# Performance work log

Hardware: AMD Instinct MI355X
Metric: run time of the kernel (lower is better)

The kernel has to match this reference:

```python
import jax, jax.numpy as jnp
import numpy as np

N_NODES = 500_000
N_EDGES = 5_000_000


def _glorot(key, shape):
    fan_in, fan_out = shape[0], shape[1]
    s = jnp.sqrt(6.0 / (fan_in + fan_out))
    return jax.random.uniform(key, shape, jnp.float32, -s, s)


def setup_inputs() -> dict:
    key = jax.random.key(0)
    ks = jax.random.split(key, 16)
    x = jax.random.normal(ks[0], (N_NODES, 3), jnp.float32)
    edge_index = jax.random.randint(ks[1], (2, N_EDGES), 0, N_NODES, jnp.int64)
    dims = [(3, 16), (16, 16), (16, 1)]
    inp = {"x": x, "edge_index": edge_index}
    for i, (din, dout) in enumerate(dims, start=1):
        k = jax.random.split(ks[1 + i], 5)
        inp[f"p{i}_w"] = _glorot(k[0], (din, din))   # project lin (bias=True)
        inp[f"p{i}_b"] = jnp.zeros((din,), jnp.float32)
        inp[f"l{i}_w"] = _glorot(k[1], (din, dout))  # lin_l on aggregated neighbors (bias=True)
        inp[f"l{i}_b"] = jnp.zeros((dout,), jnp.float32)
        inp[f"r{i}_w"] = _glorot(k[2], (din, dout))  # lin_r on root (bias=False)
    return inp


def _sage_conv(x, src, dst, pw, pb, lw, lb, rw):
    # project=True: neighbor messages use relu(lin(x)); root term uses original x
    h = jax.nn.relu(x @ pw + pb)                    # [N, din]
    msg = jnp.take(h, src, axis=0)                  # [E, din] gather from source j
    agg = jax.ops.segment_sum(msg, dst, num_segments=N_NODES)  # scatter-add to target i
    return agg @ lw + lb + x @ rw                   # [N, dout]


def reference(x, edge_index, p1_w, p1_b, l1_w, l1_b, r1_w,
              p2_w, p2_b, l2_w, l2_b, r2_w,
              p3_w, p3_b, l3_w, l3_b, r3_w):
    src, dst = edge_index[0], edge_index[1]
    h = jax.nn.relu(_sage_conv(x, src, dst, p1_w, p1_b, l1_w, l1_b, r1_w))
    h = jax.nn.relu(_sage_conv(h, src, dst, p2_w, p2_b, l2_w, l2_b, r2_w))
    return jax.nn.sigmoid(_sage_conv(h, src, dst, p3_w, p3_b, l3_w, l3_b, r3_w))
```

## Files before the change

### kernel.cpp

```cpp
#include <hip/hip_runtime.h>
#include <hip/hip_fp16.h>
#include <math.h>

#define NN 500000
#define NE 5000000
#define K_B 977
#define NBP 500
#define EPB 10000
#define CAP 6144
#define SEG 3072
#define PH 16
#define PHW 31250

__device__ inline float2 cvt2(unsigned u) {
    __half2 h = *reinterpret_cast<const __half2*>(&u);
    return __half22float2(h);
}

__device__ inline int wave_iscan(int x, int lane) {
#pragma unroll
    for (int d = 1; d < 64; d <<= 1) {
        int u = __shfl_up(x, d);
        if (lane >= d) x += u;
    }
    return x;
}


__global__ __launch_bounds__(512) void part_kernel(
    const int* __restrict__ ei, int* __restrict__ counts,
    unsigned int* __restrict__ edg_staged,
    const float* __restrict__ x, const float* __restrict__ p1w,
    const float* __restrict__ p1b, __half* __restrict__ h1)
{
    __shared__ unsigned stage[EPB];
    __shared__ int hist[1024];
    __shared__ int wsum[8];
    int t = threadIdx.x, j = blockIdx.x;
    int e0 = j * EPB;
    hist[t] = 0; hist[t + 512] = 0;
    __syncthreads();
    for (int k = t; k < EPB; k += 512) {
        int d = ei[NE + e0 + k];
        atomicAdd(&hist[d >> 9], 1);
    }
    __syncthreads();
    int v0 = hist[2*t], v1 = hist[2*t+1];
    int sv2 = v0 + v1;
    int lane = t & 63, w = t >> 6;
    int inc = wave_iscan(sv2, lane);
    if (lane == 63) wsum[w] = inc;
    __syncthreads();
    if (t == 0) {
        int run = 0;
#pragma unroll
        for (int i = 0; i < 8; ++i) { int tm = wsum[i]; wsum[i] = run; run += tm; }
    }
    __syncthreads();
    int excl = inc - sv2 + wsum[w];
    hist[2*t] = excl;
    hist[2*t+1] = excl + v0;
    if (2*t < K_B)   counts[j*K_B + 2*t]   = excl;
    if (2*t+1 < K_B) counts[j*K_B + 2*t+1] = excl + v0;
    __syncthreads();
    for (int k = t; k < EPB; k += 512) {
        int e = e0 + k;
        int sv = ei[e];
        int d = ei[NE + e];
        int pos = atomicAdd(&hist[d >> 9], 1);
        stage[pos] = ((unsigned)(d & 511) << 20) | (unsigned)sv;
    }
    __syncthreads();
    for (int k = t; k < EPB; k += 512)
        edg_staged[e0 + k] = stage[k];
    for (int i = j * 1000 + t; i < j * 1000 + 1000; i += 512) {
        float x0 = x[i*3+0], x1 = x[i*3+1], x2v = x[i*3+2];
        __half hh[4];
#pragma unroll
        for (int jj = 0; jj < 3; ++jj) {
            float v = fmaf(x0, p1w[0*3+jj], fmaf(x1, p1w[1*3+jj], fmaf(x2v, p1w[2*3+jj], p1b[jj])));
            hh[jj] = __float2half(v > 0.f ? v : 0.f);
        }
        hh[3] = __float2half(0.f);
        *reinterpret_cast<uint2*>(h1 + (size_t)i * 4) = *reinterpret_cast<uint2*>(hh);
    }
}


__global__ __launch_bounds__(512, 4) void csrfin_l1(
    const int* __restrict__ counts,
    const unsigned int* __restrict__ edg_staged,
    const __half* __restrict__ h1, const float* __restrict__ x,
    const float* __restrict__ l1w, const float* __restrict__ l1b,
    const float* __restrict__ r1w,
    const float* __restrict__ p2w, const float* __restrict__ p2b,
    unsigned int* __restrict__ edg_fin, unsigned int* __restrict__ rowptr,
    __half* __restrict__ X2, __half* __restrict__ H2)
{
    __shared__ unsigned ebuf[CAP];
    __shared__ unsigned ebuf2[CAP];
    __shared__ int cnt[512];
    __shared__ int wsum[8];
    __shared__ int sh_total;
    __shared__ float slw[48], srw[48], slb[16], sp2w[256], sp2b[16];
    int b = blockIdx.x, t = threadIdx.x;
    if (t < 256) sp2w[t] = p2w[t];
    if (t < 48) { slw[t] = l1w[t]; srw[t] = r1w[t]; }
    if (t < 16) { slb[t] = l1b[t]; sp2b[t] = p2b[t]; }
    int pj = 0, lj = 0;
    if (t < NBP) {
        int base = t * K_B;
        int w0 = counts[base + b];
        int nx = (b == K_B - 1) ? EPB : counts[base + b + 1];
        pj = t * EPB + w0;
        lj = nx - w0;
    }
    int lane = t & 63, w = t >> 6;
    int inc = wave_iscan(lj, lane);
    if (lane == 63) wsum[w] = inc;
    __syncthreads();
    if (t == 0) {
        int run = 0;
#pragma unroll
        for (int i = 0; i < 8; ++i) { int tm = wsum[i]; wsum[i] = run; run += tm; }
        sh_total = run;
    }
    __syncthreads();
    int poff = inc - lj + wsum[w];
    {
        int k = 0;
        for (; k + 4 <= lj; k += 4) {
            unsigned a0 = edg_staged[pj + k + 0];
            unsigned a1 = edg_staged[pj + k + 1];
            unsigned a2 = edg_staged[pj + k + 2];
            unsigned a3 = edg_staged[pj + k + 3];
            int p = poff + k;
            if (p + 3 < CAP) {
                ebuf[p + 0] = a0; ebuf[p + 1] = a1;
                ebuf[p + 2] = a2; ebuf[p + 3] = a3;
            } else {
                if (p + 0 < CAP) ebuf[p + 0] = a0;
                if (p + 1 < CAP) ebuf[p + 1] = a1;
                if (p + 2 < CAP) ebuf[p + 2] = a2;
                if (p + 3 < CAP) ebuf[p + 3] = a3;
            }
        }
        for (; k < lj; ++k) {
            int p = poff + k;
            if (p < CAP) ebuf[p] = edg_staged[pj + k];
        }
    }
    cnt[t] = 0;
    __syncthreads();
    int n2 = sh_total; if (n2 > CAP) n2 = CAP;
    for (int k = t; k < n2; k += 512) atomicAdd(&cnt[ebuf[k] >> 20], 1);
    __syncthreads();
    int myc = cnt[t];
    int inc2 = wave_iscan(myc, lane);
    if (lane == 63) wsum[w] = inc2;
    __syncthreads();
    if (t == 0) {
        int run = 0;
#pragma unroll
        for (int i = 0; i < 8; ++i) { int tm = wsum[i]; wsum[i] = run; run += tm; }
    }
    __syncthreads();
    int excl = inc2 - myc + wsum[w];
    int node = (b << 9) + t;
    unsigned gbase = (unsigned)(b * CAP + excl);
    if (node < NN) rowptr[node] = (gbase << 9) | (unsigned)myc;
    cnt[t] = excl;
    __syncthreads();
    for (int k = t; k < n2; k += 512) {
        unsigned v = ebuf[k];
        int p = atomicAdd(&cnt[v >> 20], 1);
        ebuf2[p] = v & 0xFFFFFu;
    }
    __syncthreads();
    unsigned key[32];
    bool small = (node < NN) && (myc <= 32);
    if (small) {
#pragma unroll
        for (int k = 0; k < 32; ++k) key[k] = (k < myc) ? ebuf2[excl + k] : 0xFFFFFFFFu;
#pragma unroll
        for (int kk = 2; kk <= 32; kk <<= 1) {
#pragma unroll
            for (int jj = kk >> 1; jj > 0; jj >>= 1) {
#pragma unroll
                for (int ii = 0; ii < 32; ++ii) {
                    int ix = ii ^ jj;
                    if (ix > ii) {
                        bool up = ((ii & kk) == 0);
                        unsigned a = key[ii], bb = key[ix];
                        bool sw = up ? (a > bb) : (a < bb);
                        key[ii] = sw ? bb : a;
                        key[ix] = sw ? a : bb;
                    }
                }
            }
        }
#pragma unroll
        for (int k = 0; k < 32; ++k) if (k < myc) ebuf[excl + k] = key[k];
    } else if (node < NN) {
        for (int k = 0; k < myc; ++k) {
            unsigned s = ebuf2[excl + k];
            ebuf[excl + k] = s;
            key[0] = 0;
        }
    }
    __syncthreads();
    int bbase = b * CAP;
    for (int k = t; k < n2; k += 512) edg_fin[bbase + k] = ebuf[k];
    if (node >= NN) return;
    float a0 = 0.f, a1 = 0.f, a2 = 0.f;
    if (small) {
#pragma unroll
        for (int k = 0; k < 32; ++k) if (k < myc) {
            unsigned s = key[k];
            uint2 r = *reinterpret_cast<const uint2*>(h1 + (size_t)s * 4);
            float2 p0 = cvt2(r.x), q0 = cvt2(r.y);
            a0 += p0.x; a1 += p0.y; a2 += q0.x;
        }
    } else {
        for (int k = 0; k < myc; ++k) {
            unsigned s = ebuf[excl + k];
            uint2 r = *reinterpret_cast<const uint2*>(h1 + (size_t)s * 4);
            float2 p0 = cvt2(r.x), q0 = cvt2(r.y);
            a0 += p0.x; a1 += p0.y; a2 += q0.x;
        }
    }
    float x0 = x[node*3+0], x1 = x[node*3+1], x2v = x[node*3+2];
    float h[16];
#pragma unroll
    for (int j = 0; j < 16; ++j) {
        float v = slb[j];
        v = fmaf(a0, slw[j], fmaf(a1, slw[16+j], fmaf(a2, slw[32+j], v)));
        v = fmaf(x0, srw[j], fmaf(x1, srw[16+j], fmaf(x2v, srw[32+j], v)));
        h[j] = v > 0.f ? v : 0.f;
    }
    __half hx[16];
#pragma unroll
    for (int j = 0; j < 16; ++j) hx[j] = __float2half(h[j]);
    uint4* xp = reinterpret_cast<uint4*>(X2 + (size_t)node * 16);
    xp[0] = reinterpret_cast<uint4*>(hx)[0];
    xp[1] = reinterpret_cast<uint4*>(hx)[1];
    __half hh[16];
#pragma unroll
    for (int j = 0; j < 16; ++j) {
        float v = sp2b[j];
#pragma unroll
        for (int k = 0; k < 16; ++k) v = fmaf(h[k], sp2w[k*16+j], v);
        hh[j] = __float2half(v > 0.f ? v : 0.f);
    }
    uint4* hp = reinterpret_cast<uint4*>(H2 + (size_t)node * 16);
    hp[0] = reinterpret_cast<uint4*>(hh)[0];
    hp[1] = reinterpret_cast<uint4*>(hh)[1];
}


__global__ __launch_bounds__(256, 8) void layer2_kernel(
    const unsigned int* __restrict__ rowptr, const unsigned int* __restrict__ edg,
    const __half* __restrict__ H2, __half* X ,
    const float* __restrict__ l2w, const float* __restrict__ l2b,
    const float* __restrict__ r2w,
    const float* __restrict__ p3w, const float* __restrict__ p3b,
    const float* __restrict__ l3w, __half* __restrict__ g)
{
    __shared__ float slw[256], srw[256], sp3w[256];
    __shared__ float slb[16], sp3b[16], sl3w[16];
    __shared__ unsigned sedg[SEG];
    __shared__ int sred[256];
    int t = threadIdx.x;
    slw[t] = l2w[t]; srw[t] = r2w[t]; sp3w[t] = p3w[t];
    if (t < 16) { slb[t] = l2b[t]; sp3b[t] = p3b[t]; sl3w[t] = l3w[t]; }
    int i = blockIdx.x * 256 + t;
    bool act = i < NN;
    unsigned rp = act ? rowptr[i] : 0;
    int beg = (int)(rp >> 9), deg = act ? (int)(rp & 511u) : 0;
    sred[t] = act ? (beg + deg) : 0;
    __syncthreads();
    int base = (int)(rowptr[blockIdx.x * 256] >> 9);
    for (int off = 128; off > 0; off >>= 1) {
        if (t < off) { int o = sred[t + off]; if (o > sred[t]) sred[t] = o; }
        __syncthreads();
    }
    int seglen = sred[0] - base;
    if (seglen > SEG) seglen = SEG;
    for (int k = t; k < seglen; k += 256) sedg[k] = edg[base + k];
    __syncthreads();
    int e = beg - base, eend = e + deg;
    if (eend > SEG) eend = SEG;
    float av[16];
#pragma unroll
    for (int k = 0; k < 16; ++k) av[k] = 0.f;
#pragma unroll 1
    for (int p = 1; p <= PH; ++p) {
        unsigned lim = (unsigned)(p * PHW);
        while (e < eend) {
            unsigned s0 = sedg[e];
            if (s0 >= lim) break;
            const uint4* r0 = reinterpret_cast<const uint4*>(H2 + (size_t)s0 * 16);
            uint4 A0 = r0[0], B0 = r0[1];
            float2 f;
            f = cvt2(A0.x); av[0] += f.x; av[1] += f.y;
            f = cvt2(A0.y); av[2] += f.x; av[3] += f.y;
            f = cvt2(A0.z); av[4] += f.x; av[5] += f.y;
            f = cvt2(A0.w); av[6] += f.x; av[7] += f.y;
            f = cvt2(B0.x); av[8] += f.x; av[9] += f.y;
            f = cvt2(B0.y); av[10] += f.x; av[11] += f.y;
            f = cvt2(B0.z); av[12] += f.x; av[13] += f.y;
            f = cvt2(B0.w); av[14] += f.x; av[15] += f.y;
            ++e;
        }
        __syncthreads();
    }
    if (!act) return;
    float xv[16];
    const uint4* xp = reinterpret_cast<const uint4*>(X + (size_t)i * 16);
    uint4 XA = xp[0], XB = xp[1];
    {
        float2 f;
        f = cvt2(XA.x); xv[0] = f.x; xv[1] = f.y;
        f = cvt2(XA.y); xv[2] = f.x; xv[3] = f.y;
        f = cvt2(XA.z); xv[4] = f.x; xv[5] = f.y;
        f = cvt2(XA.w); xv[6] = f.x; xv[7] = f.y;
        f = cvt2(XB.x); xv[8] = f.x; xv[9] = f.y;
        f = cvt2(XB.y); xv[10] = f.x; xv[11] = f.y;
        f = cvt2(XB.z); xv[12] = f.x; xv[13] = f.y;
        f = cvt2(XB.w); xv[14] = f.x; xv[15] = f.y;
    }
    float o[16];
#pragma unroll
    for (int j = 0; j < 16; ++j) {
        float v = slb[j];
#pragma unroll
        for (int k = 0; k < 16; ++k) v = fmaf(av[k], slw[k*16+j], v);
#pragma unroll
        for (int k = 0; k < 16; ++k) v = fmaf(xv[k], srw[k*16+j], v);
        o[j] = v > 0.f ? v : 0.f;
    }
    __half ho[16];
#pragma unroll
    for (int j = 0; j < 16; ++j) ho[j] = __float2half(o[j]);
    uint4* op = reinterpret_cast<uint4*>(X + (size_t)i * 16);
    op[0] = reinterpret_cast<uint4*>(ho)[0];
    op[1] = reinterpret_cast<uint4*>(ho)[1];
    float gg = 0.f;
#pragma unroll
    for (int j = 0; j < 16; ++j) {
        float u = sp3b[j];
#pragma unroll
        for (int k = 0; k < 16; ++k) u = fmaf(o[k], sp3w[k*16+j], u);
        u = u > 0.f ? u : 0.f;
        gg = fmaf(u, sl3w[j], gg);
    }
    g[i] = __float2half(gg);
}


__global__ __launch_bounds__(256) void layer3_kernel(
    const unsigned int* __restrict__ rowptr, const unsigned int* __restrict__ edg,
    const __half* __restrict__ g, const __half* __restrict__ X,
    const float* __restrict__ l3b, const float* __restrict__ r3w,
    float* __restrict__ out)
{
    __shared__ float srw[16];
    __shared__ float sb;
    int t = threadIdx.x;
    if (t < 16) srw[t] = r3w[t];
    if (t == 0) sb = l3b[0];
    __syncthreads();
    int i = blockIdx.x * 256 + t;
    if (i >= NN) return;
    unsigned rp = rowptr[i];
    int beg = (int)(rp >> 9), deg = (int)(rp & 511u);
    int end = beg + deg;
    float a = 0.f;
    int e = beg;
    for (; e + 1 < end; e += 2) {
        int s0 = (int)edg[e], s1 = (int)edg[e+1];
        __half g0 = g[s0], g1 = g[s1];
        a += __half2float(g0) + __half2float(g1);
    }
    if (e < end) a += __half2float(g[(int)edg[e]]);
    float val = a + sb;
    const uint4* xp = reinterpret_cast<const uint4*>(X + (size_t)i * 16);
    uint4 XA = xp[0], XB = xp[1];
    float2 f;
    f = cvt2(XA.x); val = fmaf(f.x, srw[0], fmaf(f.y, srw[1], val));
    f = cvt2(XA.y); val = fmaf(f.x, srw[2], fmaf(f.y, srw[3], val));
    f = cvt2(XA.z); val = fmaf(f.x, srw[4], fmaf(f.y, srw[5], val));
    f = cvt2(XA.w); val = fmaf(f.x, srw[6], fmaf(f.y, srw[7], val));
    f = cvt2(XB.x); val = fmaf(f.x, srw[8], fmaf(f.y, srw[9], val));
    f = cvt2(XB.y); val = fmaf(f.x, srw[10], fmaf(f.y, srw[11], val));
    f = cvt2(XB.z); val = fmaf(f.x, srw[12], fmaf(f.y, srw[13], val));
    f = cvt2(XB.w); val = fmaf(f.x, srw[14], fmaf(f.y, srw[15], val));
    out[i] = 1.f / (1.f + expf(-val));
}


extern "C" void kernel_launch(void* const* d_in, const int* in_sizes, int n_in,
                              void* d_out, int out_size, void* d_ws, size_t ws_size,
                              hipStream_t stream) {
    const float* x   = (const float*)d_in[0];
    const int*   ei  = (const int*)d_in[1];
    const float* p1w = (const float*)d_in[2];
    const float* p1b = (const float*)d_in[3];
    const float* l1w = (const float*)d_in[4];
    const float* l1b = (const float*)d_in[5];
    const float* r1w = (const float*)d_in[6];
    const float* p2w = (const float*)d_in[7];
    const float* p2b = (const float*)d_in[8];
    const float* l2w = (const float*)d_in[9];
    const float* l2b = (const float*)d_in[10];
    const float* r2w = (const float*)d_in[11];
    const float* p3w = (const float*)d_in[12];
    const float* p3b = (const float*)d_in[13];
    const float* l3w = (const float*)d_in[14];
    const float* l3b = (const float*)d_in[15];
    const float* r3w = (const float*)d_in[16];
    float* out = (float*)d_out;

    char* ws = (char*)d_ws;
    __half*       X        = (__half*)(ws);
    __half*       H2       = (__half*)(ws + 16000000);
    unsigned int* edg_stg  = (unsigned int*)(ws + 32000000);
    unsigned int* edg_fin  = (unsigned int*)(ws + 52000000);
    __half*       h1       = (__half*)(ws + 76012288);
    __half*       g        = (__half*)(ws + 80012288);
    unsigned int* rowptr   = (unsigned int*)(ws + 81012288);
    int*          counts   = (int*)(ws + 83012288);

    const int nbN = (NN + 255) / 256;

    part_kernel<<<NBP, 512, 0, stream>>>(ei, counts, edg_stg, x, p1w, p1b, h1);
    csrfin_l1<<<K_B, 512, 0, stream>>>(counts, edg_stg, h1, x,
                                       l1w, l1b, r1w, p2w, p2b,
                                       edg_fin, rowptr, X, H2);
    layer2_kernel<<<nbN, 256, 0, stream>>>(rowptr, edg_fin, H2, X,
                                           l2w, l2b, r2w, p3w, p3b, l3w, g);
    layer3_kernel<<<nbN, 256, 0, stream>>>(rowptr, edg_fin, g, X, l3b, r3w, out);
}
```

Measured before the change: 182.4 us.

## Replace per-row bitonic sort with 16-bucket coarse counting sort by source

The per-destination bitonic sort of up to 32 source indices is replaced by a finer counting sort. Edges are binned by (destination, top bits of source), so each row ends up grouped into 16 coarse source ranges instead of fully sorted. Two 16-bit counters are packed per shared-memory word to keep the histogram in 4096 words. This removes the register-heavy sorting network and the separate path for large rows, while still giving the gathers some locality. In exchange, neighbours within a bucket are not fully ordered, and the launch bound on occupancy is dropped; PHW also changes to a power of two.

```diff
diff --git a/kernel.cpp b/kernel.cpp
--- a/kernel.cpp
+++ b/kernel.cpp
@@ -10,7 +10,7 @@
 #define CAP 6144
 #define SEG 3072
 #define PH 16
-#define PHW 31250
+#define PHW 32768
 
 __device__ inline float2 cvt2(unsigned u) {
     __half2 h = *reinterpret_cast<const __half2*>(&u);
@@ -87,7 +87,7 @@
 }
 
 
-__global__ __launch_bounds__(512, 4) void csrfin_l1(
+__global__ __launch_bounds__(512) void csrfin_l1(
     const int* __restrict__ counts,
     const unsigned int* __restrict__ edg_staged,
     const __half* __restrict__ h1, const float* __restrict__ x,
@@ -99,7 +99,7 @@
 {
     __shared__ unsigned ebuf[CAP];
     __shared__ unsigned ebuf2[CAP];
-    __shared__ int cnt[512];
+    __shared__ unsigned cnt[4096];
     __shared__ int wsum[8];
     __shared__ int sh_total;
     __shared__ float slw[48], srw[48], slb[16], sp2w[256], sp2b[16];
@@ -125,6 +125,8 @@
         for (int i = 0; i < 8; ++i) { int tm = wsum[i]; wsum[i] = run; run += tm; }
         sh_total = run;
     }
+    cnt[t] = 0; cnt[t + 512] = 0; cnt[t + 1024] = 0; cnt[t + 1536] = 0;
+    cnt[t + 2048] = 0; cnt[t + 2560] = 0; cnt[t + 3072] = 0; cnt[t + 3584] = 0;
     __syncthreads();
     int poff = inc - lj + wsum[w];
     {
@@ -150,12 +152,20 @@
             if (p < CAP) ebuf[p] = edg_staged[pj + k];
         }
     }
-    cnt[t] = 0;
     __syncthreads();
     int n2 = sh_total; if (n2 > CAP) n2 = CAP;
-    for (int k = t; k < n2; k += 512) atomicAdd(&cnt[ebuf[k] >> 20], 1);
-    __syncthreads();
-    int myc = cnt[t];
+    for (int k = t; k < n2; k += 512) {
+        unsigned v = ebuf[k];
+        unsigned bin = ((v >> 20) << 4) | ((v & 0xFFFFFu) >> 15);
+        atomicAdd(&cnt[bin >> 1], (bin & 1u) ? 65536u : 1u);
+    }
+    __syncthreads();
+    unsigned wlo[8];
+#pragma unroll
+    for (int q = 0; q < 8; ++q) wlo[q] = cnt[t * 8 + q];
+    int myc = 0;
+#pragma unroll
+    for (int q = 0; q < 8; ++q) myc += (int)(wlo[q] & 0xFFFFu) + (int)(wlo[q] >> 16);
     int inc2 = wave_iscan(myc, lane);
     if (lane == 63) wsum[w] = inc2;
     __syncthreads();
@@ -169,65 +179,34 @@
     int node = (b << 9) + t;
     unsigned gbase = (unsigned)(b * CAP + excl);
     if (node < NN) rowptr[node] = (gbase << 9) | (unsigned)myc;
-    cnt[t] = excl;
+    {
+        int run2 = excl;
+#pragma unroll
+        for (int q = 0; q < 8; ++q) {
+            int c0 = (int)(wlo[q] & 0xFFFFu), c1 = (int)(wlo[q] >> 16);
+            cnt[t * 8 + q] = (unsigned)run2 | ((unsigned)(run2 + c0) << 16);
+            run2 += c0 + c1;
+        }
+    }
     __syncthreads();
     for (int k = t; k < n2; k += 512) {
         unsigned v = ebuf[k];
-        int p = atomicAdd(&cnt[v >> 20], 1);
-        ebuf2[p] = v & 0xFFFFFu;
-    }
-    __syncthreads();
-    unsigned key[32];
-    bool small = (node < NN) && (myc <= 32);
-    if (small) {
-#pragma unroll
-        for (int k = 0; k < 32; ++k) key[k] = (k < myc) ? ebuf2[excl + k] : 0xFFFFFFFFu;
-#pragma unroll
-        for (int kk = 2; kk <= 32; kk <<= 1) {
-#pragma unroll
-            for (int jj = kk >> 1; jj > 0; jj >>= 1) {
-#pragma unroll
-                for (int ii = 0; ii < 32; ++ii) {
-                    int ix = ii ^ jj;
-                    if (ix > ii) {
-                        bool up = ((ii & kk) == 0);
-                        unsigned a = key[ii], bb = key[ix];
-                        bool sw = up ? (a > bb) : (a < bb);
-                        key[ii] = sw ? bb : a;
-                        key[ix] = sw ? a : bb;
-                    }
-                }
-            }
-        }
-#pragma unroll
-        for (int k = 0; k < 32; ++k) if (k < myc) ebuf[excl + k] = key[k];
-    } else if (node < NN) {
-        for (int k = 0; k < myc; ++k) {
-            unsigned s = ebuf2[excl + k];
-            ebuf[excl + k] = s;
-            key[0] = 0;
-        }
+        unsigned src = v & 0xFFFFFu;
+        unsigned bin = ((v >> 20) << 4) | (src >> 15);
+        unsigned old = atomicAdd(&cnt[bin >> 1], (bin & 1u) ? 65536u : 1u);
+        unsigned pos = (bin & 1u) ? (old >> 16) : (old & 0xFFFFu);
+        ebuf2[pos] = src;
     }
     __syncthreads();
     int bbase = b * CAP;
-    for (int k = t; k < n2; k += 512) edg_fin[bbase + k] = ebuf[k];
+    for (int k = t; k < n2; k += 512) edg_fin[bbase + k] = ebuf2[k];
     if (node >= NN) return;
     float a0 = 0.f, a1 = 0.f, a2 = 0.f;
-    if (small) {
-#pragma unroll
-        for (int k = 0; k < 32; ++k) if (k < myc) {
-            unsigned s = key[k];
-            uint2 r = *reinterpret_cast<const uint2*>(h1 + (size_t)s * 4);
-            float2 p0 = cvt2(r.x), q0 = cvt2(r.y);
-            a0 += p0.x; a1 += p0.y; a2 += q0.x;
-        }
-    } else {
-        for (int k = 0; k < myc; ++k) {
-            unsigned s = ebuf[excl + k];
-            uint2 r = *reinterpret_cast<const uint2*>(h1 + (size_t)s * 4);
-            float2 p0 = cvt2(r.x), q0 = cvt2(r.y);
-            a0 += p0.x; a1 += p0.y; a2 += q0.x;
-        }
+    for (int k = 0; k < myc; ++k) {
+        unsigned s = ebuf2[excl + k];
+        uint2 r = *reinterpret_cast<const uint2*>(h1 + (size_t)s * 4);
+        float2 p0 = cvt2(r.x), q0 = cvt2(r.y);
+        a0 += p0.x; a1 += p0.y; a2 += q0.x;
     }
     float x0 = x[node*3+0], x1 = x[node*3+1], x2v = x[node*3+2];
     float h[16];
```

New measurement: 178.8 us. 2.0% less time.
